# Performance work log

Measured on AMD Instinct MI355X. Metric: run time of the kernel, lower is better.

The kernel has to match this reference:

```python
import jax, jax.numpy as jnp
import numpy as np

EPS = 1e-5

def _layer_norm(x, g, b):
    mu = jnp.mean(x, axis=-1, keepdims=True)
    var = jnp.mean(jnp.square(x - mu), axis=-1, keepdims=True)
    return (x - mu) * jax.lax.rsqrt(var + EPS) * g + b

def setup_inputs() -> dict:
    key = jax.random.key(0)
    ks = jax.random.split(key, 8)
    B, N, M = 4, 2048, 2048
    Dq, Dc = 512, 768
    H, Dh = 8, 64
    inner = H * Dh  # 512
    s = lambda d: 1.0 / np.sqrt(d)
    return {
        "x": jax.random.normal(ks[0], (B, N, Dq), jnp.float32),
        "cond": jax.random.normal(ks[1], (B, M, Dc), jnp.float32),
        "lnx_g": jnp.ones((Dq,), jnp.float32),
        "lnx_b": jnp.zeros((Dq,), jnp.float32),
        "lnc_g": jnp.ones((Dc,), jnp.float32),
        "lnc_b": jnp.zeros((Dc,), jnp.float32),
        "Wq": jax.random.normal(ks[2], (Dq, inner), jnp.float32) * s(Dq),
        "Wk": jax.random.normal(ks[3], (Dc, inner), jnp.float32) * s(Dc),
        "Wv": jax.random.normal(ks[4], (Dc, inner), jnp.float32) * s(Dc),
        "Wo": jax.random.normal(ks[5], (inner, Dq), jnp.float32) * s(inner),
        "bo": jnp.zeros((Dq,), jnp.float32),
        "lnf_g": jnp.ones((Dq,), jnp.float32),
        "lnf_b": jnp.zeros((Dq,), jnp.float32),
    }

def reference(x, cond, lnx_g, lnx_b, lnc_g, lnc_b, Wq, Wk, Wv, Wo, bo, lnf_g, lnf_b):
    H = 8
    B, N, _ = x.shape
    M = cond.shape[1]
    x_orig = x
    xn = _layer_norm(x, lnx_g, lnx_b)
    cn = _layer_norm(cond, lnc_g, lnc_b)
    q = (xn @ Wq).reshape(B, N, H, -1).transpose(0, 2, 1, 3)  # b h n d
    k = (cn @ Wk).reshape(B, M, H, -1).transpose(0, 2, 1, 3)  # b h m d
    v = (cn @ Wv).reshape(B, M, H, -1).transpose(0, 2, 1, 3)
    scale = q.shape[-1] ** -0.5
    sim = jnp.einsum('bhid,bhjd->bhij', q, k) * scale
    attn = jax.nn.softmax(sim, axis=-1)
    out = jnp.einsum('bhij,bhjd->bhid', attn, v)
    out = out.transpose(0, 2, 1, 3).reshape(B, N, -1)  # b n (h d)
    out = out @ Wo + bo
    out = out + x_orig  # residual=True
    return _layer_norm(out, lnf_g, lnf_b)
```

## Files before the change

### kernel.cpp

```cpp
#include <hip/hip_runtime.h>
#include <hip/hip_bf16.h>
#include <math.h>

#define BB 4
#define NN 2048
#define MM 2048
#define DQ 512
#define DC 768
#define NH 8
#define DH 64
#define INNER 512
#define KVS 1024

typedef short bf16x8 __attribute__((ext_vector_type(8)));
typedef short bf16x4 __attribute__((ext_vector_type(4)));
typedef float f32x4  __attribute__((ext_vector_type(4)));

__device__ inline short fbf(float f) {
    __hip_bfloat16 h = __float2bfloat16(f);
    return __builtin_bit_cast(short, h);
}

__device__ inline void gld16(const void* gptr, void* lds_uniform_base) {
    __builtin_amdgcn_global_load_lds(
        (const __attribute__((address_space(1))) void*)gptr,
        (__attribute__((address_space(3))) void*)lds_uniform_base, 16, 0, 0);
}

__global__ __launch_bounds__(256) void prep_k(
    const float* __restrict__ x, const float* __restrict__ cond,
    const float* __restrict__ gx, const float* __restrict__ bx_,
    const float* __restrict__ gc, const float* __restrict__ bc,
    short* __restrict__ xn, short* __restrict__ cn,
    const float* __restrict__ Wq, const float* __restrict__ Wk,
    const float* __restrict__ Wv, const float* __restrict__ Wo,
    short* __restrict__ Wqt, short* __restrict__ Wkvt, short* __restrict__ Wot)
{
    const int bxid = blockIdx.x;
    const int t = threadIdx.x;

    if (bxid < 16384) {
        const int which = bxid >> 13;
        const int row   = bxid & 8191;
        const float* in = which ? cond : x;
        const float* g  = which ? gc : gx;
        const float* bb = which ? bc : bx_;
        short* out      = which ? cn : xn;
        const int D     = which ? DC : DQ;

        const float* xr = in + (size_t)row * D;
        float s = 0.f, s2 = 0.f;
        for (int d = t; d < D; d += 256) {
            float v = xr[d];
            s += v; s2 += v * v;
        }
        __shared__ float red[2][4];
        #pragma unroll
        for (int off = 32; off; off >>= 1) {
            s  += __shfl_down(s,  off, 64);
            s2 += __shfl_down(s2, off, 64);
        }
        const int wave = t >> 6, lane = t & 63;
        if (lane == 0) { red[0][wave] = s; red[1][wave] = s2; }
        __syncthreads();
        if (t == 0) {
            float ts = red[0][0] + red[0][1] + red[0][2] + red[0][3];
            float t2 = red[1][0] + red[1][1] + red[1][2] + red[1][3];
            float mu = ts / (float)D;
            float var = t2 / (float)D - mu * mu;
            red[0][0] = mu;
            red[1][0] = rsqrtf(var + 1e-5f);
        }
        __syncthreads();
        const float mu = red[0][0], rstd = red[1][0];
        short* o = out + (size_t)row * D;
        for (int d = t; d < D; d += 256)
            o[d] = fbf((xr[d] - mu) * rstd * g[d] + bb[d]);
    } else {
        const int tb = bxid - 16384;
        const int y = tb >> 4;
        const int n0 = (tb & 15) * 32;
        const float* W; short* Wt; int K, k0;
        if (y < 16)      { W = Wq; Wt = Wqt;  K = DQ; k0 = y * 32; }
        else if (y < 40) { W = Wk; Wt = Wkvt; K = DC; k0 = (y - 16) * 32; }
        else if (y < 64) { W = Wv; Wt = Wkvt + (size_t)512 * DC; K = DC; k0 = (y - 40) * 32; }
        else             { W = Wo; Wt = Wot;  K = DQ; k0 = (y - 64) * 32; }

        __shared__ float tile[32][33];
        const int r = t >> 3, c4 = (t & 7) * 4;
        float4 vv = *(const float4*)&W[(size_t)(k0 + r) * 512 + n0 + c4];
        tile[c4 + 0][r] = vv.x; tile[c4 + 1][r] = vv.y;
        tile[c4 + 2][r] = vv.z; tile[c4 + 3][r] = vv.w;
        __syncthreads();
        short4 sv;
        sv.x = fbf(tile[r][c4 + 0]); sv.y = fbf(tile[r][c4 + 1]);
        sv.z = fbf(tile[r][c4 + 2]); sv.w = fbf(tile[r][c4 + 3]);
        *(short4*)&Wt[(size_t)(n0 + r) * K + k0 + c4] = sv;
    }
}

__global__ __launch_bounds__(256) void layernorm_res_f32(
    const short* __restrict__ ob, const float* __restrict__ x,
    const float* __restrict__ g, const float* __restrict__ b,
    float* __restrict__ out)
{
    const int row = blockIdx.x;
    const int t = threadIdx.x;
    const size_t base = (size_t)row * DQ;
    float v0, v1;
    {
        unsigned u0 = (unsigned)(unsigned short)ob[base + t];
        unsigned u1 = (unsigned)(unsigned short)ob[base + t + 256];
        v0 = __builtin_bit_cast(float, u0 << 16) + x[base + t];
        v1 = __builtin_bit_cast(float, u1 << 16) + x[base + t + 256];
    }
    float s = v0 + v1, s2 = v0 * v0 + v1 * v1;
    __shared__ float red[2][4];
    #pragma unroll
    for (int off = 32; off; off >>= 1) {
        s  += __shfl_down(s,  off, 64);
        s2 += __shfl_down(s2, off, 64);
    }
    const int wave = t >> 6, lane = t & 63;
    if (lane == 0) { red[0][wave] = s; red[1][wave] = s2; }
    __syncthreads();
    if (t == 0) {
        float ts = red[0][0] + red[0][1] + red[0][2] + red[0][3];
        float t2 = red[1][0] + red[1][1] + red[1][2] + red[1][3];
        float mu = ts / (float)DQ;
        float var = t2 / (float)DQ - mu * mu;
        red[0][0] = mu;
        red[1][0] = rsqrtf(var + 1e-5f);
    }
    __syncthreads();
    const float mu = red[0][0], rstd = red[1][0];
    out[base + t]       = (v0 - mu) * rstd * g[t]       + b[t];
    out[base + t + 256] = (v1 - mu) * rstd * g[t + 256] + b[t + 256];
}

#define GBK 32

__global__ __launch_bounds__(256) void qkv_gemm(
    const short* __restrict__ xn, const short* __restrict__ cn,
    const short* __restrict__ Wqt, const short* __restrict__ Wkvt,
    short* __restrict__ qb, short* __restrict__ kvb, float qsc)
{
    const short* A; const short* Bt; short* outp; int K, Nout, n0; float sc;
    if (blockIdx.x < 4) {
        A = xn; Bt = Wqt; outp = qb; K = DQ; Nout = 512;
        n0 = blockIdx.x * 128; sc = qsc;
    } else {
        A = cn; Bt = Wkvt; outp = kvb; K = DC; Nout = 1024;
        n0 = (blockIdx.x - 4) * 128; sc = 1.f;
    }
    __shared__ short As[128 * GBK];
    __shared__ short Bs[128 * GBK];
    const int t = threadIdx.x;
    const int w = t >> 6, lane = t & 63;
    const int quad = lane >> 4, l16 = lane & 15;
    const int m0 = blockIdx.y * 128;
    const int wm = (w >> 1) * 64, wn = (w & 1) * 64;

    f32x4 acc[4][4];
    #pragma unroll
    for (int i = 0; i < 4; ++i)
        #pragma unroll
        for (int j = 0; j < 4; ++j) acc[i][j] = (f32x4){0.f, 0.f, 0.f, 0.f};

    for (int kt = 0; kt < K; kt += GBK) {
        __syncthreads();
        #pragma unroll
        for (int i = 0; i < 2; ++i) {
            const int j = w * 2 + i;
            const int c = j * 64 + lane;
            gld16(&A[(size_t)(m0 + (c >> 2)) * K + kt + (c & 3) * 8],
                  (char*)As + j * 1024);
            gld16(&Bt[(size_t)(n0 + (c >> 2)) * K + kt + (c & 3) * 8],
                  (char*)Bs + j * 1024);
        }
        __syncthreads();

        bf16x8 af[4], bfr[4];
        #pragma unroll
        for (int mt = 0; mt < 4; ++mt)
            af[mt] = *(bf16x8*)&As[(wm + mt * 16 + l16) * GBK + quad * 8];
        #pragma unroll
        for (int nt = 0; nt < 4; ++nt)
            bfr[nt] = *(bf16x8*)&Bs[(wn + nt * 16 + l16) * GBK + quad * 8];
        #pragma unroll
        for (int mt = 0; mt < 4; ++mt)
            #pragma unroll
            for (int nt = 0; nt < 4; ++nt)
                acc[mt][nt] = __builtin_amdgcn_mfma_f32_16x16x32_bf16(
                    af[mt], bfr[nt], acc[mt][nt], 0, 0, 0);
    }

    #pragma unroll
    for (int mt = 0; mt < 4; ++mt)
        #pragma unroll
        for (int r = 0; r < 4; ++r) {
            const int m = m0 + wm + mt * 16 + quad * 4 + r;
            #pragma unroll
            for (int nt = 0; nt < 4; ++nt) {
                const int n = n0 + wn + nt * 16 + l16;
                outp[(size_t)m * Nout + n] = fbf(acc[mt][nt][r] * sc);
            }
        }
}

__global__ __launch_bounds__(256) void oproj_gemm(
    const short* __restrict__ A, const short* __restrict__ Bt,
    short* __restrict__ outb, const float* __restrict__ bias)
{
    const int K = INNER, Nout = INNER;
    __shared__ short As[128 * GBK];
    __shared__ short Bs[64 * GBK];
    const int t = threadIdx.x;
    const int w = t >> 6, lane = t & 63;
    const int quad = lane >> 4, l16 = lane & 15;
    const int m0 = blockIdx.y * 128, n0 = blockIdx.x * 64;
    const int wm = (w >> 1) * 64, wn = (w & 1) * 32;

    f32x4 acc[4][2];
    #pragma unroll
    for (int i = 0; i < 4; ++i)
        #pragma unroll
        for (int j = 0; j < 2; ++j) acc[i][j] = (f32x4){0.f, 0.f, 0.f, 0.f};

    for (int kt = 0; kt < K; kt += GBK) {
        __syncthreads();
        #pragma unroll
        for (int i = 0; i < 2; ++i) {
            const int j = w * 2 + i;
            const int c = j * 64 + lane;
            gld16(&A[(size_t)(m0 + (c >> 2)) * K + kt + (c & 3) * 8],
                  (char*)As + j * 1024);
        }
        {
            const int c = w * 64 + lane;
            gld16(&Bt[(size_t)(n0 + (c >> 2)) * K + kt + (c & 3) * 8],
                  (char*)Bs + w * 1024);
        }
        __syncthreads();

        bf16x8 af[4], bfr[2];
        #pragma unroll
        for (int mt = 0; mt < 4; ++mt)
            af[mt] = *(bf16x8*)&As[(wm + mt * 16 + l16) * GBK + quad * 8];
        #pragma unroll
        for (int nt = 0; nt < 2; ++nt)
            bfr[nt] = *(bf16x8*)&Bs[(wn + nt * 16 + l16) * GBK + quad * 8];
        #pragma unroll
        for (int mt = 0; mt < 4; ++mt)
            #pragma unroll
            for (int nt = 0; nt < 2; ++nt)
                acc[mt][nt] = __builtin_amdgcn_mfma_f32_16x16x32_bf16(
                    af[mt], bfr[nt], acc[mt][nt], 0, 0, 0);
    }

    #pragma unroll
    for (int mt = 0; mt < 4; ++mt)
        #pragma unroll
        for (int r = 0; r < 4; ++r) {
            const int m = m0 + wm + mt * 16 + quad * 4 + r;
            #pragma unroll
            for (int nt = 0; nt < 2; ++nt) {
                const int n = n0 + wn + nt * 16 + l16;
                outb[(size_t)m * Nout + n] = fbf(acc[mt][nt][r] + bias[n]);
            }
        }
}

#define QT 64
#define JT 32
#define MH (MM / 2)
#define NIT (MH / JT)
#define ABUF 16384

__global__ __launch_bounds__(512, 6) void attention_mfma(
    const short* __restrict__ q, const short* __restrict__ kv,
    short* __restrict__ o)
{
    const int bid = blockIdx.x;
    const int wg  = (bid & 7) * 128 + (bid >> 3);
    const int ib  = wg & 31;
    const int bh  = wg >> 5;
    const int h   = bh & 7, b = bh >> 3;
    const int i0  = ib * QT;

    const int t = threadIdx.x;
    const int wave = t >> 6, lane = t & 63;
    const int w4 = wave & 3, hh = wave >> 2;
    const int quad = lane >> 4, l16 = lane & 15;

    __shared__ __align__(16) char smem[2 * ABUF];

    const int qrow = i0 + w4 * 16 + l16;
    const short* qp = &q[((size_t)(b * NN + qrow)) * INNER + h * DH];
    const bf16x8 qf0 = *(const bf16x8*)&qp[quad * 8];
    const bf16x8 qf1 = *(const bf16x8*)&qp[32 + quad * 8];

    f32x4 Oa[4];
    f32x4 La = (f32x4){0.f, 0.f, 0.f, 0.f};
    #pragma unroll
    for (int dt = 0; dt < 4; ++dt) Oa[dt] = (f32x4){0.f, 0.f, 0.f, 0.f};

    const bf16x8 ones8 = {(short)0x3F80, (short)0x3F80, (short)0x3F80, (short)0x3F80,
                          (short)0x3F80, (short)0x3F80, (short)0x3F80, (short)0x3F80};

    const int kr = w4 * 8 + (lane >> 3);
    const int kc = ((lane & 7) ^ (lane >> 3)) * 8;
    const short* kp = kv + ((size_t)(b * MM + hh * MH + kr)) * KVS + h * DH + kc;
    const int vj = (lane >> 3) * 4 + ((lane & 7) >> 1);
    const int vd = w4 * 16 + (lane & 1) * 8;
    const short* vp = kv + ((size_t)(b * MM + hh * MH + vj)) * KVS + 512 + h * DH + vd;
    const size_t ADV = (size_t)JT * KVS;

    char* const kdst = smem + hh * 4096 + w4 * 1024;
    char* const vdst = smem + 8192 + hh * 4096 + w4 * 1024;

    const char* const Kh0 = smem + hh * 4096;
    const int koffA = l16 * 128 + ((quad ^ (l16 & 7)) * 16);
    const int koffB = koffA ^ 64;
    const unsigned vbase =
        (unsigned)(size_t)(__attribute__((address_space(3))) char*)(smem + 8192 + hh * 4096)
        + (unsigned)(lane * 8);

    auto stage = [&](int pb) {
        gld16(kp, kdst + pb);
        gld16(vp, vdst + pb);
        kp += ADV; vp += ADV;
    };

    auto compute = [&](int pb) {
        const char* Kh = Kh0 + pb;
        bf16x8 kf0 = *(const bf16x8*)(Kh + koffA);
        bf16x8 kf1 = *(const bf16x8*)(Kh + koffB);
        bf16x8 kg0 = *(const bf16x8*)(Kh + koffA + 2048);
        bf16x8 kg1 = *(const bf16x8*)(Kh + koffB + 2048);
        f32x4 Sc0 = (f32x4){0.f, 0.f, 0.f, 0.f};
        f32x4 Sc1 = (f32x4){0.f, 0.f, 0.f, 0.f};
        Sc0 = __builtin_amdgcn_mfma_f32_16x16x32_bf16(kf0, qf0, Sc0, 0, 0, 0);
        Sc0 = __builtin_amdgcn_mfma_f32_16x16x32_bf16(kf1, qf1, Sc0, 0, 0, 0);
        Sc1 = __builtin_amdgcn_mfma_f32_16x16x32_bf16(kg0, qf0, Sc1, 0, 0, 0);
        Sc1 = __builtin_amdgcn_mfma_f32_16x16x32_bf16(kg1, qf1, Sc1, 0, 0, 0);

        bf16x4 ta0, tb0, ta1, tb1, ta2, tb2, ta3, tb3;
        {
            const unsigned va = vbase + (unsigned)pb;
            asm volatile(
                "ds_read_b64_tr_b16 %0, %8 offset:0\n\t"
                "ds_read_b64_tr_b16 %1, %8 offset:512\n\t"
                "ds_read_b64_tr_b16 %2, %8 offset:1024\n\t"
                "ds_read_b64_tr_b16 %3, %8 offset:1536\n\t"
                "ds_read_b64_tr_b16 %4, %8 offset:2048\n\t"
                "ds_read_b64_tr_b16 %5, %8 offset:2560\n\t"
                "ds_read_b64_tr_b16 %6, %8 offset:3072\n\t"
                "ds_read_b64_tr_b16 %7, %8 offset:3584"
                : "=&v"(ta0), "=&v"(tb0), "=&v"(ta1), "=&v"(tb1),
                  "=&v"(ta2), "=&v"(tb2), "=&v"(ta3), "=&v"(tb3)
                : "v"(va));
        }

        const float e0 = exp2f(Sc0[0]), e1 = exp2f(Sc0[1]);
        const float e2 = exp2f(Sc0[2]), e3 = exp2f(Sc0[3]);
        const float f0 = exp2f(Sc1[0]), f1 = exp2f(Sc1[1]);
        const float f2 = exp2f(Sc1[2]), f3 = exp2f(Sc1[3]);
        uint4 pk;
        pk.x = __builtin_amdgcn_perm(__builtin_bit_cast(unsigned, e1),
                                     __builtin_bit_cast(unsigned, e0), 0x07060302u);
        pk.y = __builtin_amdgcn_perm(__builtin_bit_cast(unsigned, e3),
                                     __builtin_bit_cast(unsigned, e2), 0x07060302u);
        pk.z = __builtin_amdgcn_perm(__builtin_bit_cast(unsigned, f1),
                                     __builtin_bit_cast(unsigned, f0), 0x07060302u);
        pk.w = __builtin_amdgcn_perm(__builtin_bit_cast(unsigned, f3),
                                     __builtin_bit_cast(unsigned, f2), 0x07060302u);
        const bf16x8 p8 = __builtin_bit_cast(bf16x8, pk);

        asm volatile("s_waitcnt lgkmcnt(0)" ::: "memory");
        __builtin_amdgcn_sched_barrier(0);

        const bf16x8 v0 = __builtin_shufflevector(ta0, tb0, 0, 1, 2, 3, 4, 5, 6, 7);
        const bf16x8 v1 = __builtin_shufflevector(ta1, tb1, 0, 1, 2, 3, 4, 5, 6, 7);
        const bf16x8 v2 = __builtin_shufflevector(ta2, tb2, 0, 1, 2, 3, 4, 5, 6, 7);
        const bf16x8 v3 = __builtin_shufflevector(ta3, tb3, 0, 1, 2, 3, 4, 5, 6, 7);
        Oa[0] = __builtin_amdgcn_mfma_f32_16x16x32_bf16(p8, v0, Oa[0], 0, 0, 0);
        Oa[1] = __builtin_amdgcn_mfma_f32_16x16x32_bf16(p8, v1, Oa[1], 0, 0, 0);
        Oa[2] = __builtin_amdgcn_mfma_f32_16x16x32_bf16(p8, v2, Oa[2], 0, 0, 0);
        Oa[3] = __builtin_amdgcn_mfma_f32_16x16x32_bf16(p8, v3, Oa[3], 0, 0, 0);
        La    = __builtin_amdgcn_mfma_f32_16x16x32_bf16(p8, ones8, La, 0, 0, 0);
    };

    stage(0);
    __syncthreads();

    for (int itr = 0; itr < NIT; itr += 2) {
        stage(ABUF);
        compute(0);
        __syncthreads();
        if (itr + 2 < NIT) stage(0);
        compute(ABUF);
        __syncthreads();
    }

    float (*Obuf)[16][68] = (float (*)[16][68])smem;
    float (*Lbuf)[16]     = (float (*)[16])(smem + 17408);
    if (hh == 1) {
        #pragma unroll
        for (int r = 0; r < 4; ++r) {
            const int qr = quad * 4 + r;
            #pragma unroll
            for (int dt = 0; dt < 4; ++dt)
                Obuf[w4][qr][dt * 16 + l16] = Oa[dt][r];
            if (l16 == 0) Lbuf[w4][qr] = La[r];
        }
    }
    __syncthreads();
    if (hh == 0) {
        #pragma unroll
        for (int r = 0; r < 4; ++r) {
            const int qr = quad * 4 + r;
            const float ltot = La[r] + Lbuf[w4][qr];
            const float inv = 1.f / ltot;
            const int row = i0 + w4 * 16 + qr;
            #pragma unroll
            for (int dt = 0; dt < 4; ++dt) {
                const float val = Oa[dt][r] + Obuf[w4][qr][dt * 16 + l16];
                o[((size_t)(b * NN + row)) * INNER + h * DH + dt * 16 + l16] =
                    fbf(val * inv);
            }
        }
    }
}

extern "C" void kernel_launch(void* const* d_in, const int* in_sizes, int n_in,
                              void* d_out, int out_size, void* d_ws, size_t ws_size,
                              hipStream_t stream)
{
    const float* x     = (const float*)d_in[0];
    const float* cond  = (const float*)d_in[1];
    const float* lnx_g = (const float*)d_in[2];
    const float* lnx_b = (const float*)d_in[3];
    const float* lnc_g = (const float*)d_in[4];
    const float* lnc_b = (const float*)d_in[5];
    const float* Wq    = (const float*)d_in[6];
    const float* Wk    = (const float*)d_in[7];
    const float* Wv    = (const float*)d_in[8];
    const float* Wo    = (const float*)d_in[9];
    const float* bo    = (const float*)d_in[10];
    const float* lnf_g = (const float*)d_in[11];
    const float* lnf_b = (const float*)d_in[12];
    float* out = (float*)d_out;
    char* ws = (char*)d_ws;

    const int R = BB * NN;

    short* xn_bf  = (short*)(ws);
    short* cn_bf  = (short*)(ws + (8u << 20));
    short* Wq_t   = (short*)(ws + (20u << 20));
    short* Wo_t   = (short*)(ws + (21u << 20));
    short* Wkv_t  = (short*)(ws + (22u << 20));
    short* qb     = (short*)(ws + (24u << 20));
    short* kvb    = (short*)(ws + (32u << 20));
    short* ab     = (short*)(ws + (48u << 20));
    short* ob     = (short*)(ws + (56u << 20));

    prep_k<<<17664, 256, 0, stream>>>(
        x, cond, lnx_g, lnx_b, lnc_g, lnc_b, xn_bf, cn_bf,
        Wq, Wk, Wv, Wo, Wq_t, Wkv_t, Wo_t);

    qkv_gemm<<<dim3(12, R / 128), 256, 0, stream>>>(
        xn_bf, cn_bf, Wq_t, Wkv_t, qb, kvb, 0.125f * 1.44269504089f);

    attention_mfma<<<dim3(BB * NH * (NN / QT)), 512, 0, stream>>>(qb, kvb, ab);

    oproj_gemm<<<dim3(INNER / 64, R / 128), 256, 0, stream>>>(ab, Wo_t, ob, bo);

    layernorm_res_f32<<<R, 256, 0, stream>>>(ob, x, lnf_g, lnf_b, out);
}
```

Measured before the change: 226.3 us.

## Enlarge attention tiles and use one wave per row in layernorms

The attention kernel now gives each wave two 16-row query tiles (128 query rows per block) and stages 64 keys per iteration, so every K/V fragment read from LDS feeds twice as many MFMAs and the grid halves. Occupancy drops to 4 blocks per CU and register pressure rises. Both layernorm kernels change from one 256-thread block per row to one wave per row, using float4 loads and xor-shuffle reductions, which removes the shared-memory reductions and block barriers. The larger tile leaves fewer blocks for the GPU to spread across its compute units, a possible tail effect.

Result: faster. 209.6 us (-7.4%).

```diff
diff --git a/kernel.cpp b/kernel.cpp
--- a/kernel.cpp
+++ b/kernel.cpp
@@ -19,6 +19,10 @@
 __device__ inline short fbf(float f) {
     __hip_bfloat16 h = __float2bfloat16(f);
     return __builtin_bit_cast(short, h);
+}
+__device__ inline float bf2f(short s) {
+    unsigned u = (unsigned)(unsigned short)s;
+    return __builtin_bit_cast(float, u << 16);
 }
 
 __device__ inline void gld16(const void* gptr, void* lds_uniform_base) {
@@ -39,45 +43,54 @@
     const int bxid = blockIdx.x;
     const int t = threadIdx.x;
 
-    if (bxid < 16384) {
-        const int which = bxid >> 13;
-        const int row   = bxid & 8191;
+    if (bxid < 4096) {
+        const int which = bxid >> 11;
+        const int wave = t >> 6, lane = t & 63;
+        const int row = (bxid & 2047) * 4 + wave;
         const float* in = which ? cond : x;
         const float* g  = which ? gc : gx;
         const float* bb = which ? bc : bx_;
         short* out      = which ? cn : xn;
         const int D     = which ? DC : DQ;
+        const int nk    = which ? 3 : 2;
 
         const float* xr = in + (size_t)row * D;
+        float v[12];
         float s = 0.f, s2 = 0.f;
-        for (int d = t; d < D; d += 256) {
-            float v = xr[d];
-            s += v; s2 += v * v;
-        }
-        __shared__ float red[2][4];
+        #pragma unroll
+        for (int k = 0; k < 3; ++k) {
+            if (k < nk) {
+                float4 f = *(const float4*)&xr[lane * 4 + k * 256];
+                v[k * 4 + 0] = f.x; v[k * 4 + 1] = f.y;
+                v[k * 4 + 2] = f.z; v[k * 4 + 3] = f.w;
+                s  += f.x + f.y + f.z + f.w;
+                s2 += f.x * f.x + f.y * f.y + f.z * f.z + f.w * f.w;
+            }
+        }
         #pragma unroll
         for (int off = 32; off; off >>= 1) {
-            s  += __shfl_down(s,  off, 64);
-            s2 += __shfl_down(s2, off, 64);
-        }
-        const int wave = t >> 6, lane = t & 63;
-        if (lane == 0) { red[0][wave] = s; red[1][wave] = s2; }
-        __syncthreads();
-        if (t == 0) {
-            float ts = red[0][0] + red[0][1] + red[0][2] + red[0][3];
-            float t2 = red[1][0] + red[1][1] + red[1][2] + red[1][3];
-            float mu = ts / (float)D;
-            float var = t2 / (float)D - mu * mu;
-            red[0][0] = mu;
-            red[1][0] = rsqrtf(var + 1e-5f);
-        }
-        __syncthreads();
-        const float mu = red[0][0], rstd = red[1][0];
+            s  += __shfl_xor(s,  off, 64);
+            s2 += __shfl_xor(s2, off, 64);
+        }
+        const float mu = s / (float)D;
+        const float rstd = rsqrtf(s2 / (float)D - mu * mu + 1e-5f);
         short* o = out + (size_t)row * D;
-        for (int d = t; d < D; d += 256)
-            o[d] = fbf((xr[d] - mu) * rstd * g[d] + bb[d]);
+        #pragma unroll
+        for (int k = 0; k < 3; ++k) {
+            if (k < nk) {
+                const int d = lane * 4 + k * 256;
+                float4 gg = *(const float4*)&g[d];
+                float4 bv = *(const float4*)&bb[d];
+                short4 sv;
+                sv.x = fbf((v[k * 4 + 0] - mu) * rstd * gg.x + bv.x);
+                sv.y = fbf((v[k * 4 + 1] - mu) * rstd * gg.y + bv.y);
+                sv.z = fbf((v[k * 4 + 2] - mu) * rstd * gg.z + bv.z);
+                sv.w = fbf((v[k * 4 + 3] - mu) * rstd * gg.w + bv.w);
+                *(short4*)&o[d] = sv;
+            }
+        }
     } else {
-        const int tb = bxid - 16384;
+        const int tb = bxid - 4096;
         const int y = tb >> 4;
         const int n0 = (tb & 15) * 32;
         const float* W; short* Wt; int K, k0;
@@ -104,38 +117,41 @@
     const float* __restrict__ g, const float* __restrict__ b,
     float* __restrict__ out)
 {
-    const int row = blockIdx.x;
-    const int t = threadIdx.x;
+    const int wave = threadIdx.x >> 6, lane = threadIdx.x & 63;
+    const int row = blockIdx.x * 4 + wave;
     const size_t base = (size_t)row * DQ;
-    float v0, v1;
-    {
-        unsigned u0 = (unsigned)(unsigned short)ob[base + t];
-        unsigned u1 = (unsigned)(unsigned short)ob[base + t + 256];
-        v0 = __builtin_bit_cast(float, u0 << 16) + x[base + t];
-        v1 = __builtin_bit_cast(float, u1 << 16) + x[base + t + 256];
-    }
-    float s = v0 + v1, s2 = v0 * v0 + v1 * v1;
-    __shared__ float red[2][4];
+    float v[8];
+    float s = 0.f, s2 = 0.f;
+    #pragma unroll
+    for (int k = 0; k < 2; ++k) {
+        const int d = lane * 4 + k * 256;
+        short4 ov = *(const short4*)&ob[base + d];
+        float4 xv = *(const float4*)&x[base + d];
+        float a0 = bf2f(ov.x) + xv.x, a1 = bf2f(ov.y) + xv.y;
+        float a2 = bf2f(ov.z) + xv.z, a3 = bf2f(ov.w) + xv.w;
+        v[k * 4 + 0] = a0; v[k * 4 + 1] = a1; v[k * 4 + 2] = a2; v[k * 4 + 3] = a3;
+        s  += a0 + a1 + a2 + a3;
+        s2 += a0 * a0 + a1 * a1 + a2 * a2 + a3 * a3;
+    }
     #pragma unroll
     for (int off = 32; off; off >>= 1) {
-        s  += __shfl_down(s,  off, 64);
-        s2 += __shfl_down(s2, off, 64);
-    }
-    const int wave = t >> 6, lane = t & 63;
-    if (lane == 0) { red[0][wave] = s; red[1][wave] = s2; }
-    __syncthreads();
-    if (t == 0) {
-        float ts = red[0][0] + red[0][1] + red[0][2] + red[0][3];
-        float t2 = red[1][0] + red[1][1] + red[1][2] + red[1][3];
-        float mu = ts / (float)DQ;
-        float var = t2 / (float)DQ - mu * mu;
-        red[0][0] = mu;
-        red[1][0] = rsqrtf(var + 1e-5f);
-    }
-    __syncthreads();
-    const float mu = red[0][0], rstd = red[1][0];
-    out[base + t]       = (v0 - mu) * rstd * g[t]       + b[t];
-    out[base + t + 256] = (v1 - mu) * rstd * g[t + 256] + b[t + 256];
+        s  += __shfl_xor(s,  off, 64);
+        s2 += __shfl_xor(s2, off, 64);
+    }
+    const float mu = s / (float)DQ;
+    const float rstd = rsqrtf(s2 / (float)DQ - mu * mu + 1e-5f);
+    #pragma unroll
+    for (int k = 0; k < 2; ++k) {
+        const int d = lane * 4 + k * 256;
+        float4 gv = *(const float4*)&g[d];
+        float4 bv = *(const float4*)&b[d];
+        float4 r;
+        r.x = (v[k * 4 + 0] - mu) * rstd * gv.x + bv.x;
+        r.y = (v[k * 4 + 1] - mu) * rstd * gv.y + bv.y;
+        r.z = (v[k * 4 + 2] - mu) * rstd * gv.z + bv.z;
+        r.w = (v[k * 4 + 3] - mu) * rstd * gv.w + bv.w;
+        *(float4*)&out[base + d] = r;
+    }
 }
 
 #define GBK 32
@@ -271,44 +287,53 @@
         }
 }
 
-#define QT 64
-#define JT 32
+#define QT 128
+#define JT 64
 #define MH (MM / 2)
 #define NIT (MH / JT)
-#define ABUF 16384
-
-__global__ __launch_bounds__(512, 6) void attention_mfma(
+#define ABUF 32768
+
+__global__ __launch_bounds__(512, 4) void attention_mfma(
     const short* __restrict__ q, const short* __restrict__ kv,
     short* __restrict__ o)
 {
     const int bid = blockIdx.x;
-    const int wg  = (bid & 7) * 128 + (bid >> 3);
-    const int ib  = wg & 31;
-    const int bh  = wg >> 5;
+    const int wg  = (bid & 7) * 64 + (bid >> 3);
+    const int ib  = wg & 15;
+    const int bh  = wg >> 4;
     const int h   = bh & 7, b = bh >> 3;
     const int i0  = ib * QT;
 
     const int t = threadIdx.x;
-    const int wave = t >> 6, lane = t & 63;
+    const int lane = t & 63;
+    const int wave = t >> 6;
     const int w4 = wave & 3, hh = wave >> 2;
     const int quad = lane >> 4, l16 = lane & 15;
 
     __shared__ __align__(16) char smem[2 * ABUF];
 
-    const int qrow = i0 + w4 * 16 + l16;
-    const short* qp = &q[((size_t)(b * NN + qrow)) * INNER + h * DH];
-    const bf16x8 qf0 = *(const bf16x8*)&qp[quad * 8];
-    const bf16x8 qf1 = *(const bf16x8*)&qp[32 + quad * 8];
-
-    f32x4 Oa[4];
-    f32x4 La = (f32x4){0.f, 0.f, 0.f, 0.f};
-    #pragma unroll
-    for (int dt = 0; dt < 4; ++dt) Oa[dt] = (f32x4){0.f, 0.f, 0.f, 0.f};
+    bf16x8 qf[2][2];
+    #pragma unroll
+    for (int it = 0; it < 2; ++it) {
+        const int qrow = i0 + w4 * 32 + it * 16 + l16;
+        const short* qp = &q[((size_t)(b * NN + qrow)) * INNER + h * DH];
+        qf[it][0] = *(const bf16x8*)&qp[quad * 8];
+        qf[it][1] = *(const bf16x8*)&qp[32 + quad * 8];
+    }
+
+    f32x4 Oa[2][4];
+    f32x4 La[2];
+    #pragma unroll
+    for (int it = 0; it < 2; ++it) {
+        La[it] = (f32x4){0.f, 0.f, 0.f, 0.f};
+        #pragma unroll
+        for (int dt = 0; dt < 4; ++dt) Oa[it][dt] = (f32x4){0.f, 0.f, 0.f, 0.f};
+    }
 
     const bf16x8 ones8 = {(short)0x3F80, (short)0x3F80, (short)0x3F80, (short)0x3F80,
                           (short)0x3F80, (short)0x3F80, (short)0x3F80, (short)0x3F80};
 
-    const int kr = w4 * 8 + (lane >> 3);
+    const int kr = w4 * 16 + (lane >> 3);
     const int kc = ((lane & 7) ^ (lane >> 3)) * 8;
     const short* kp = kv + ((size_t)(b * MM + hh * MH + kr)) * KVS + h * DH + kc;
     const int vj = (lane >> 3) * 4 + ((lane & 7) >> 1);
@@ -316,79 +341,115 @@
     const short* vp = kv + ((size_t)(b * MM + hh * MH + vj)) * KVS + 512 + h * DH + vd;
     const size_t ADV = (size_t)JT * KVS;
 
-    char* const kdst = smem + hh * 4096 + w4 * 1024;
-    char* const vdst = smem + 8192 + hh * 4096 + w4 * 1024;
-
-    const char* const Kh0 = smem + hh * 4096;
-    const int koffA = l16 * 128 + ((quad ^ (l16 & 7)) * 16);
-    const int koffB = koffA ^ 64;
+    char* const kdst = smem + hh * 8192 + w4 * 2048;
+    char* const vdst = smem + 16384 + hh * 8192 + w4 * 2048;
+
+    const char* const Kh0 = smem + hh * 8192;
+    const int koff0 = l16 * 128 + ((quad ^ (l16 & 7)) * 16);
     const unsigned vbase =
-        (unsigned)(size_t)(__attribute__((address_space(3))) char*)(smem + 8192 + hh * 4096)
+        (unsigned)(size_t)(__attribute__((address_space(3))) char*)(smem + 16384 + hh * 8192)
         + (unsigned)(lane * 8);
 
     auto stage = [&](int pb) {
-        gld16(kp, kdst + pb);
-        gld16(vp, vdst + pb);
+        gld16(kp,            kdst + pb);
+        gld16(kp + 8 * KVS,  kdst + pb + 1024);
+        gld16(vp,            vdst + pb);
+        gld16(vp + 32 * KVS, vdst + pb + 1024);
         kp += ADV; vp += ADV;
     };
 
     auto compute = [&](int pb) {
         const char* Kh = Kh0 + pb;
-        bf16x8 kf0 = *(const bf16x8*)(Kh + koffA);
-        bf16x8 kf1 = *(const bf16x8*)(Kh + koffB);
-        bf16x8 kg0 = *(const bf16x8*)(Kh + koffA + 2048);
-        bf16x8 kg1 = *(const bf16x8*)(Kh + koffB + 2048);
-        f32x4 Sc0 = (f32x4){0.f, 0.f, 0.f, 0.f};
-        f32x4 Sc1 = (f32x4){0.f, 0.f, 0.f, 0.f};
-        Sc0 = __builtin_amdgcn_mfma_f32_16x16x32_bf16(kf0, qf0, Sc0, 0, 0, 0);
-        Sc0 = __builtin_amdgcn_mfma_f32_16x16x32_bf16(kf1, qf1, Sc0, 0, 0, 0);
-        Sc1 = __builtin_amdgcn_mfma_f32_16x16x32_bf16(kg0, qf0, Sc1, 0, 0, 0);
-        Sc1 = __builtin_amdgcn_mfma_f32_16x16x32_bf16(kg1, qf1, Sc1, 0, 0, 0);
-
-        bf16x4 ta0, tb0, ta1, tb1, ta2, tb2, ta3, tb3;
-        {
-            const unsigned va = vbase + (unsigned)pb;
-            asm volatile(
-                "ds_read_b64_tr_b16 %0, %8 offset:0\n\t"
-                "ds_read_b64_tr_b16 %1, %8 offset:512\n\t"
-                "ds_read_b64_tr_b16 %2, %8 offset:1024\n\t"
-                "ds_read_b64_tr_b16 %3, %8 offset:1536\n\t"
-                "ds_read_b64_tr_b16 %4, %8 offset:2048\n\t"
-                "ds_read_b64_tr_b16 %5, %8 offset:2560\n\t"
-                "ds_read_b64_tr_b16 %6, %8 offset:3072\n\t"
-                "ds_read_b64_tr_b16 %7, %8 offset:3584"
-                : "=&v"(ta0), "=&v"(tb0), "=&v"(ta1), "=&v"(tb1),
-                  "=&v"(ta2), "=&v"(tb2), "=&v"(ta3), "=&v"(tb3)
-                : "v"(va));
-        }
-
-        const float e0 = exp2f(Sc0[0]), e1 = exp2f(Sc0[1]);
-        const float e2 = exp2f(Sc0[2]), e3 = exp2f(Sc0[3]);
-        const float f0 = exp2f(Sc1[0]), f1 = exp2f(Sc1[1]);
-        const float f2 = exp2f(Sc1[2]), f3 = exp2f(Sc1[3]);
-        uint4 pk;
-        pk.x = __builtin_amdgcn_perm(__builtin_bit_cast(unsigned, e1),
-                                     __builtin_bit_cast(unsigned, e0), 0x07060302u);
-        pk.y = __builtin_amdgcn_perm(__builtin_bit_cast(unsigned, e3),
-                                     __builtin_bit_cast(unsigned, e2), 0x07060302u);
-        pk.z = __builtin_amdgcn_perm(__builtin_bit_cast(unsigned, f1),
-                                     __builtin_bit_cast(unsigned, f0), 0x07060302u);
-        pk.w = __builtin_amdgcn_perm(__builtin_bit_cast(unsigned, f3),
-                                     __builtin_bit_cast(unsigned, f2), 0x07060302u);
-        const bf16x8 p8 = __builtin_bit_cast(bf16x8, pk);
-
-        asm volatile("s_waitcnt lgkmcnt(0)" ::: "memory");
-        __builtin_amdgcn_sched_barrier(0);
-
-        const bf16x8 v0 = __builtin_shufflevector(ta0, tb0, 0, 1, 2, 3, 4, 5, 6, 7);
-        const bf16x8 v1 = __builtin_shufflevector(ta1, tb1, 0, 1, 2, 3, 4, 5, 6, 7);
-        const bf16x8 v2 = __builtin_shufflevector(ta2, tb2, 0, 1, 2, 3, 4, 5, 6, 7);
-        const bf16x8 v3 = __builtin_shufflevector(ta3, tb3, 0, 1, 2, 3, 4, 5, 6, 7);
-        Oa[0] = __builtin_amdgcn_mfma_f32_16x16x32_bf16(p8, v0, Oa[0], 0, 0, 0);
-        Oa[1] = __builtin_amdgcn_mfma_f32_16x16x32_bf16(p8, v1, Oa[1], 0, 0, 0);
-        Oa[2] = __builtin_amdgcn_mfma_f32_16x16x32_bf16(p8, v2, Oa[2], 0, 0, 0);
-        Oa[3] = __builtin_amdgcn_mfma_f32_16x16x32_bf16(p8, v3, Oa[3], 0, 0, 0);
-        La    = __builtin_amdgcn_mfma_f32_16x16x32_bf16(p8, ones8, La, 0, 0, 0);
+        #pragma unroll
+        for (int cc = 0; cc < 2; ++cc) {
+            const int kb = cc * 4096 + koff0;
+            bf16x8 kf0 = *(const bf16x8*)(Kh + kb);
+            bf16x8 kf1 = *(const bf16x8*)(Kh + (kb ^ 64));
+            bf16x8 kg0 = *(const bf16x8*)(Kh + kb + 2048);
+            bf16x8 kg1 = *(const bf16x8*)(Kh + ((kb + 2048) ^ 64));
+
+            f32x4 S00 = (f32x4){0.f, 0.f, 0.f, 0.f};
+            f32x4 S01 = (f32x4){0.f, 0.f, 0.f, 0.f};
+            f32x4 S10 = (f32x4){0.f, 0.f, 0.f, 0.f};
+            f32x4 S11 = (f32x4){0.f, 0.f, 0.f, 0.f};
+            S00 = __builtin_amdgcn_mfma_f32_16x16x32_bf16(kf0, qf[0][0], S00, 0, 0, 0);
+            S00 = __builtin_amdgcn_mfma_f32_16x16x32_bf16(kf1, qf[0][1], S00, 0, 0, 0);
+            S01 = __builtin_amdgcn_mfma_f32_16x16x32_bf16(kf0, qf[1][0], S01, 0, 0, 0);
+            S01 = __builtin_amdgcn_mfma_f32_16x16x32_bf16(kf1, qf[1][1], S01, 0, 0, 0);
+            S10 = __builtin_amdgcn_mfma_f32_16x16x32_bf16(kg0, qf[0][0], S10, 0, 0, 0);
+            S10 = __builtin_amdgcn_mfma_f32_16x16x32_bf16(kg1, qf[0][1], S10, 0, 0, 0);
+            S11 = __builtin_amdgcn_mfma_f32_16x16x32_bf16(kg0, qf[1][0], S11, 0, 0, 0);
+            S11 = __builtin_amdgcn_mfma_f32_16x16x32_bf16(kg1, qf[1][1], S11, 0, 0, 0);
+
+            bf16x4 ta0, tb0, ta1, tb1, ta2, tb2, ta3, tb3;
+            {
+                const unsigned va = vbase + (unsigned)(cc * 1024 + pb);
+                asm volatile(
+                    "ds_read_b64_tr_b16 %0, %8 offset:0\n\t"
+                    "ds_read_b64_tr_b16 %1, %8 offset:512\n\t"
+                    "ds_read_b64_tr_b16 %2, %8 offset:2048\n\t"
+                    "ds_read_b64_tr_b16 %3, %8 offset:2560\n\t"
+                    "ds_read_b64_tr_b16 %4, %8 offset:4096\n\t"
+                    "ds_read_b64_tr_b16 %5, %8 offset:4608\n\t"
+                    "ds_read_b64_tr_b16 %6, %8 offset:6144\n\t"
+                    "ds_read_b64_tr_b16 %7, %8 offset:6656"
+                    : "=&v"(ta0), "=&v"(tb0), "=&v"(ta1), "=&v"(tb1),
+                      "=&v"(ta2), "=&v"(tb2), "=&v"(ta3), "=&v"(tb3)
+                    : "v"(va));
+            }
+
+            bf16x8 p8[2];
+            {
+                const float e0 = exp2f(S00[0]), e1 = exp2f(S00[1]);
+                const float e2 = exp2f(S00[2]), e3 = exp2f(S00[3]);
+                const float f0 = exp2f(S10[0]), f1 = exp2f(S10[1]);
+                const float f2 = exp2f(S10[2]), f3 = exp2f(S10[3]);
+                uint4 pk;
+                pk.x = __builtin_amdgcn_perm(__builtin_bit_cast(unsigned, e1),
+                                             __builtin_bit_cast(unsigned, e0), 0x07060302u);
+                pk.y = __builtin_amdgcn_perm(__builtin_bit_cast(unsigned, e3),
+                                             __builtin_bit_cast(unsigned, e2), 0x07060302u);
+                pk.z = __builtin_amdgcn_perm(__builtin_bit_cast(unsigned, f1),
+                                             __builtin_bit_cast(unsigned, f0), 0x07060302u);
+                pk.w = __builtin_amdgcn_perm(__builtin_bit_cast(unsigned, f3),
+                                             __builtin_bit_cast(unsigned, f2), 0x07060302u);
+                p8[0] = __builtin_bit_cast(bf16x8, pk);
+            }
+            {
+                const float e0 = exp2f(S01[0]), e1 = exp2f(S01[1]);
+                const float e2 = exp2f(S01[2]), e3 = exp2f(S01[3]);
+                const float f0 = exp2f(S11[0]), f1 = exp2f(S11[1]);
+                const float f2 = exp2f(S11[2]), f3 = exp2f(S11[3]);
+                uint4 pk;
+                pk.x = __builtin_amdgcn_perm(__builtin_bit_cast(unsigned, e1),
+                                             __builtin_bit_cast(unsigned, e0), 0x07060302u);
+                pk.y = __builtin_amdgcn_perm(__builtin_bit_cast(unsigned, e3),
+                                             __builtin_bit_cast(unsigned, e2), 0x07060302u);
+                pk.z = __builtin_amdgcn_perm(__builtin_bit_cast(unsigned, f1),
+                                             __builtin_bit_cast(unsigned, f0), 0x07060302u);
+                pk.w = __builtin_amdgcn_perm(__builtin_bit_cast(unsigned, f3),
+                                             __builtin_bit_cast(unsigned, f2), 0x07060302u);
+                p8[1] = __builtin_bit_cast(bf16x8, pk);
+            }
+
+            asm volatile("s_waitcnt lgkmcnt(0)" ::: "memory");
+            __builtin_amdgcn_sched_barrier(0);
+
+            const bf16x8 v0 = __builtin_shufflevector(ta0, tb0, 0, 1, 2, 3, 4, 5, 6, 7);
+            const bf16x8 v1 = __builtin_shufflevector(ta1, tb1, 0, 1, 2, 3, 4, 5, 6, 7);
+            const bf16x8 v2 = __builtin_shufflevector(ta2, tb2, 0, 1, 2, 3, 4, 5, 6, 7);
+            const bf16x8 v3 = __builtin_shufflevector(ta3, tb3, 0, 1, 2, 3, 4, 5, 6, 7);
+            Oa[0][0] = __builtin_amdgcn_mfma_f32_16x16x32_bf16(p8[0], v0, Oa[0][0], 0, 0, 0);
+            Oa[0][1] = __builtin_amdgcn_mfma_f32_16x16x32_bf16(p8[0], v1, Oa[0][1], 0, 0, 0);
+            Oa[0][2] = __builtin_amdgcn_mfma_f32_16x16x32_bf16(p8[0], v2, Oa[0][2], 0, 0, 0);
+            Oa[0][3] = __builtin_amdgcn_mfma_f32_16x16x32_bf16(p8[0], v3, Oa[0][3], 0, 0, 0);
+            Oa[1][0] = __builtin_amdgcn_mfma_f32_16x16x32_bf16(p8[1], v0, Oa[1][0], 0, 0, 0);
+            Oa[1][1] = __builtin_amdgcn_mfma_f32_16x16x32_bf16(p8[1], v1, Oa[1][1], 0, 0, 0);
+            Oa[1][2] = __builtin_amdgcn_mfma_f32_16x16x32_bf16(p8[1], v2, Oa[1][2], 0, 0, 0);
+            Oa[1][3] = __builtin_amdgcn_mfma_f32_16x16x32_bf16(p8[1], v3, Oa[1][3], 0, 0, 0);
+            La[0]    = __builtin_amdgcn_mfma_f32_16x16x32_bf16(p8[0], ones8, La[0], 0, 0, 0);
+            La[1]    = __builtin_amdgcn_mfma_f32_16x16x32_bf16(p8[1], ones8, La[1], 0, 0, 0);
+        }
     };
 
     stage(0);
@@ -403,31 +464,37 @@
         __syncthreads();
     }
 
-    float (*Obuf)[16][68] = (float (*)[16][68])smem;
-    float (*Lbuf)[16]     = (float (*)[16])(smem + 17408);
+    float (*Obuf)[32][68] = (float (*)[32][68])smem;
+    float (*Lbuf)[32]     = (float (*)[32])(smem + 34816);
     if (hh == 1) {
         #pragma unroll
-        for (int r = 0; r < 4; ++r) {
-            const int qr = quad * 4 + r;
+        for (int it = 0; it < 2; ++it) {
             #pragma unroll
-            for (int dt = 0; dt < 4; ++dt)
-                Obuf[w4][qr][dt * 16 + l16] = Oa[dt][r];
-            if (l16 == 0) Lbuf[w4][qr] = La[r];
+            for (int r = 0; r < 4; ++r) {
+                const int qr = it * 16 + quad * 4 + r;
+                #pragma unroll
+                for (int dt = 0; dt < 4; ++dt)
+                    Obuf[w4][qr][dt * 16 + l16] = Oa[it][dt][r];
+                if (l16 == 0) Lbuf[w4][qr] = La[it][r];
+            }
         }
     }
     __syncthreads();
     if (hh == 0) {
         #pragma unroll
-        for (int r = 0; r < 4; ++r) {
-            const int qr = quad * 4 + r;
-            const float ltot = La[r] + Lbuf[w4][qr];
-            const float inv = 1.f / ltot;
-            const int row = i0 + w4 * 16 + qr;
+        for (int it = 0; it < 2; ++it) {
             #pragma unroll
-            for (int dt = 0; dt < 4; ++dt) {
-                const float val = Oa[dt][r] + Obuf[w4][qr][dt * 16 + l16];
-                o[((size_t)(b * NN + row)) * INNER + h * DH + dt * 16 + l16] =
-                    fbf(val * inv);
+            for (int r = 0; r < 4; ++r) {
+                const int qr = it * 16 + quad * 4 + r;
+                const float ltot = La[it][r] + Lbuf[w4][qr];
+                const float inv = 1.f / ltot;
+                const int row = i0 + w4 * 32 + qr;
+                #pragma unroll
+                for (int dt = 0; dt < 4; ++dt) {
+                    const float val = Oa[it][dt][r] + Obuf[w4][qr][dt * 16 + l16];
+                    o[((size_t)(b * NN + row)) * INNER + h * DH + dt * 16 + l16] =
+                        fbf(val * inv);
+                }
             }
         }
     }
@@ -465,7 +532,7 @@
     short* ab     = (short*)(ws + (48u << 20));
     short* ob     = (short*)(ws + (56u << 20));
 
-    prep_k<<<17664, 256, 0, stream>>>(
+    prep_k<<<5376, 256, 0, stream>>>(
         x, cond, lnx_g, lnx_b, lnc_g, lnc_b, xn_bf, cn_bf,
         Wq, Wk, Wv, Wo, Wq_t, Wkv_t, Wo_t);
 
@@ -476,5 +543,5 @@
 
     oproj_gemm<<<dim3(INNER / 64, R / 128), 256, 0, stream>>>(ab, Wo_t, ob, bo);
 
-    layernorm_res_f32<<<R, 256, 0, stream>>>(ob, x, lnf_g, lnf_b, out);
-}
+    layernorm_res_f32<<<R / 4, 256, 0, stream>>>(ob, x, lnf_g, lnf_b, out);
+}
```
